# Performance work log

Measured on AMD Instinct MI355X. Metric: run time of the kernel, lower is better.

## Reference

```python
import jax, jax.numpy as jnp
import numpy as np

B, T_MEL, T_TXT = 16, 2048, 1024
D_MODEL, D_ENC_M, D_ENC_T = 512, 512, 512
LN_EPS = 1e-5


def setup_inputs() -> dict:
    key = jax.random.key(0)
    ks = jax.random.split(key, 9)
    mel_encoding = jax.random.normal(ks[0], (B, T_MEL, D_ENC_M), dtype=jnp.float32)
    text_encoding = jax.random.normal(ks[1], (B, T_TXT, D_ENC_T), dtype=jnp.float32)
    mel_mask = jax.random.randint(ks[2], (B, T_MEL), 0, 2).astype(bool)
    mel_mask = mel_mask.at[:, 0].set(False)  # guarantee >=1 unmasked key per row
    src_mask = jax.random.randint(ks[3], (B, T_TXT), 0, 2).astype(bool)
    # Projection weights stored [in, out] (torch Linear does x @ W.T)
    sc = 1.0 / np.sqrt(D_ENC_M)
    Wq = jax.random.uniform(ks[4], (D_ENC_T, D_MODEL), jnp.float32, -sc, sc)
    Wk = jax.random.uniform(ks[5], (D_ENC_M, D_MODEL), jnp.float32, -sc, sc)
    Wv = jax.random.uniform(ks[6], (D_ENC_M, D_MODEL), jnp.float32, -sc, sc)
    ln_gamma = jnp.ones((D_MODEL,), jnp.float32)
    ln_beta = jnp.zeros((D_MODEL,), jnp.float32)
    return {"mel_encoding": mel_encoding, "text_encoding": text_encoding,
            "mel_mask": mel_mask, "src_mask": src_mask,
            "Wq": Wq, "Wk": Wk, "Wv": Wv,
            "ln_gamma": ln_gamma, "ln_beta": ln_beta}


def reference(mel_encoding, text_encoding, mel_mask, src_mask, Wq, Wk, Wv, ln_gamma, ln_beta):
    temperature = jnp.sqrt(jnp.float32(D_ENC_M))
    q = jnp.einsum('btd,dm->btm', text_encoding, Wq)   # [B, T_txt, d_model]
    k = jnp.einsum('bsd,dm->bsm', mel_encoding, Wk)    # [B, T_mel, d_model]
    v = jnp.einsum('bsd,dm->bsm', mel_encoding, Wv)
    # attn_mask = outer product of src_mask and mel_mask (True -> masked)
    attn_mask = src_mask[:, :, None] & mel_mask[:, None, :]  # [B, T_txt, T_mel]
    scores = jnp.einsum('btm,bsm->bts', q, k) / temperature
    scores = jnp.where(attn_mask, -jnp.inf, scores)
    attn = jax.nn.softmax(scores, axis=2)
    output = jnp.einsum('bts,bsm->btm', attn, v)
    # dropout is identity at inference; LayerNorm over last dim
    mean = jnp.mean(output, axis=-1, keepdims=True)
    var = jnp.var(output, axis=-1, keepdims=True)
    output = (output - mean) * jax.lax.rsqrt(var + LN_EPS) * ln_gamma + ln_beta
    return output, attn
```

## Files before the change

### kernel.cpp

```cpp
#include <hip/hip_runtime.h>

#define DEV __device__ __forceinline__

typedef __attribute__((ext_vector_type(8))) short short8v;
typedef __attribute__((ext_vector_type(4))) float f32x4;

DEV unsigned short f2bf(float f) {
  unsigned int x = __float_as_uint(f);
  x = x + 0x7FFFu + ((x >> 16) & 1u);
  return (unsigned short)(x >> 16);
}
DEV float bf2f(unsigned short u) {
  return __uint_as_float(((unsigned)u) << 16);
}

DEV int swz_byte(int row, int kElem) {
  int chunk = ((kElem >> 3) ^ (row & 7));
  return row * 128 + (chunk << 4) + ((kElem & 7) << 1);
}

template <int ROUNDS>
DEV void stage(const unsigned short* __restrict__ g, int ld,
               unsigned short* tile, int tid) {
  const int wave = tid >> 6, l = tid & 63;
#pragma unroll
  for (int p = 0; p < ROUNDS; ++p) {
    const int r = (p << 5) + (wave << 3) + (l >> 3);
    const int c = ((l & 7) ^ (r & 7)) << 3;
    const unsigned short* src = g + (long)r * ld + c;
#if __has_builtin(__builtin_amdgcn_global_load_lds)
    unsigned short* dst = tile + (p << 11) + (wave << 9);
    __builtin_amdgcn_global_load_lds(
        (const __attribute__((address_space(1))) void*)src,
        (__attribute__((address_space(3))) void*)dst, 16, 0, 0);
#else
    short8v v = *reinterpret_cast<const short8v*>(src);
    *reinterpret_cast<short8v*>(reinterpret_cast<char*>(tile) +
                                (p << 12) + (wave << 10) + (l << 4)) = v;
#endif
  }
}

template <int BM, int EPI, int GM>
__global__ __launch_bounds__(256) void gemm_bf16(
    const unsigned short* __restrict__ A, const unsigned short* __restrict__ B,
    void* __restrict__ Cout, int M, int N, int K,
    long aBatch, long bBatch, long cBatch,
    const int* __restrict__ srcMask, const int* __restrict__ melMask,
    float scale, float* __restrict__ stats) {
  constexpr int NI = BM / 32;
  __shared__ unsigned short As[BM * 64];
  __shared__ unsigned short Bs[128 * 64];
  const int tid = threadIdx.x;
  const int lane = tid & 63;
  const int wave = tid >> 6;
  int z, bmi, bni;
  if constexpr (GM == 1) {
    const int id = blockIdx.x;
    z = (id & 7) | ((id >> 10) << 3);
    const int ib = (id >> 3) & 127;
    bni = ib & 15;
    bmi = ib >> 4;
  } else if constexpr (GM == 2) {
    bmi = blockIdx.x; bni = blockIdx.y; z = blockIdx.z;
  } else {
    bni = blockIdx.x; bmi = blockIdx.y; z = blockIdx.z;
  }
  const int bm = bmi * BM;
  const int bn = bni * 128;
  const unsigned short* Ab = A + (long)z * aBatch;
  const unsigned short* Bb = B + (long)z * bBatch;
  const long cOff = (long)z * cBatch;
  const int wr = (wave >> 1) * (BM / 2);
  const int wc = (wave & 1) * 64;
  const int l15 = lane & 15;
  const int lHi = lane >> 4;

  f32x4 acc[NI][4] = {};

  for (int kt = 0; kt < K; kt += 64) {
    stage<BM / 32>(Ab + (long)bm * K + kt, K, As, tid);
    stage<4>(Bb + (long)bn * K + kt, K, Bs, tid);
    __syncthreads();
#pragma unroll
    for (int ks = 0; ks < 2; ++ks) {
      const int k0 = (ks << 5) + (lHi << 3);
      short8v af[NI], bfr[4];
#pragma unroll
      for (int i = 0; i < NI; ++i)
        af[i] = *reinterpret_cast<const short8v*>(
            reinterpret_cast<const char*>(As) + swz_byte(wr + i * 16 + l15, k0));
#pragma unroll
      for (int j = 0; j < 4; ++j)
        bfr[j] = *reinterpret_cast<const short8v*>(
            reinterpret_cast<const char*>(Bs) + swz_byte(wc + j * 16 + l15, k0));
#pragma unroll
      for (int i = 0; i < NI; ++i)
#pragma unroll
        for (int j = 0; j < 4; ++j)
          acc[i][j] = __builtin_amdgcn_mfma_f32_16x16x32_bf16(af[i], bfr[j], acc[i][j], 0, 0, 0);
    }
    __syncthreads();
  }

  if constexpr (EPI >= 2) {
    __shared__ float redM[128][2];
    __shared__ float redS[128][2];
    const int wcIdx = wave & 1;
#pragma unroll
    for (int i = 0; i < NI; ++i) {
#pragma unroll
      for (int rr = 0; rr < 4; ++rr) {
        const int rloc = wr + i * 16 + lHi * 4 + rr;
        const int rb = bm + rloc;
        const bool sm = srcMask[z * 1024 + rb] != 0;
        float vals[4];
        float m_l = -3.0e38f;
#pragma unroll
        for (int j = 0; j < 4; ++j) {
          const int c = bn + wc + j * 16 + l15;
          const bool mm = melMask[z * 2048 + c] != 0;
          const float vf = (sm && mm) ? -1e30f : acc[i][j][rr] * scale;
          vals[j] = vf;
          if constexpr (EPI == 2)
            reinterpret_cast<unsigned short*>(Cout)[cOff + (long)rb * N + c] = f2bf(vf);
          else
            reinterpret_cast<float*>(Cout)[cOff + (long)rb * N + c] = vf;
          m_l = fmaxf(m_l, vf);
        }
        if (stats) {
#pragma unroll
          for (int o = 1; o < 16; o <<= 1) m_l = fmaxf(m_l, __shfl_xor(m_l, o, 64));
          float s_l = 0.f;
#pragma unroll
          for (int j = 0; j < 4; ++j) s_l += __expf(vals[j] - m_l);
#pragma unroll
          for (int o = 1; o < 16; o <<= 1) s_l += __shfl_xor(s_l, o, 64);
          if (l15 == 0) { redM[rloc][wcIdx] = m_l; redS[rloc][wcIdx] = s_l; }
        }
      }
    }
    if (stats) {
      __syncthreads();
      if (tid < 128) {
        const float m0 = redM[tid][0], m1 = redM[tid][1];
        const float Mx = fmaxf(m0, m1);
        const float S = redS[tid][0] * __expf(m0 - Mx) + redS[tid][1] * __expf(m1 - Mx);
        const long sidx = ((long)(z * 1024 + bm + tid)) * 32 + (long)bni * 2;
        stats[sidx] = Mx;
        stats[sidx + 1] = S;
      }
    }
  } else {
#pragma unroll
    for (int i = 0; i < NI; ++i) {
#pragma unroll
      for (int j = 0; j < 4; ++j) {
        const int rb = bm + wr + i * 16 + lHi * 4;
        const int c = bn + wc + j * 16 + l15;
#pragma unroll
        for (int r = 0; r < 4; ++r) {
          const float v = acc[i][j][r];
          const long idx = cOff + (long)(rb + r) * N + c;
          if constexpr (EPI == 0)
            reinterpret_cast<unsigned short*>(Cout)[idx] = f2bf(v);
          else
            reinterpret_cast<float*>(Cout)[idx] = v;
        }
      }
    }
  }
}

__global__ __launch_bounds__(256) void gemm_kv(
    const unsigned short* __restrict__ mel, const unsigned short* __restrict__ WkT,
    const unsigned short* __restrict__ WvT, unsigned short* __restrict__ kbf,
    unsigned short* __restrict__ vT) {
  __shared__ unsigned short Ms[128 * 64];
  __shared__ unsigned short Ks[128 * 64];
  __shared__ unsigned short Vs[128 * 64];
  const int id = blockIdx.x;
  const int z = (id & 7) | ((id >> 9) << 3);
  const int ib = (id >> 3) & 63;
  const int st = ib & 15, mt = ib >> 4;
  const int bs = st * 128, bmm = mt * 128;
  const int tid = threadIdx.x, lane = tid & 63, wave = tid >> 6;
  const int wrS = (wave >> 1) * 64, wcM = (wave & 1) * 64;
  const int l15 = lane & 15, lHi = lane >> 4;
  const unsigned short* melB = mel + ((long)z * 2048 + bs) * 512;

  f32x4 ak[4][4] = {};
  f32x4 av[4][4] = {};

  for (int kt = 0; kt < 512; kt += 64) {
    stage<4>(melB + kt, 512, Ms, tid);
    stage<4>(WkT + (long)bmm * 512 + kt, 512, Ks, tid);
    stage<4>(WvT + (long)bmm * 512 + kt, 512, Vs, tid);
    __syncthreads();
#pragma unroll
    for (int ks = 0; ks < 2; ++ks) {
      const int k0 = (ks << 5) + (lHi << 3);
      short8v mf[4], wf[4];
#pragma unroll
      for (int i = 0; i < 4; ++i)
        mf[i] = *reinterpret_cast<const short8v*>(
            reinterpret_cast<const char*>(Ms) + swz_byte(wrS + i * 16 + l15, k0));
#pragma unroll
      for (int j = 0; j < 4; ++j)
        wf[j] = *reinterpret_cast<const short8v*>(
            reinterpret_cast<const char*>(Ks) + swz_byte(wcM + j * 16 + l15, k0));
#pragma unroll
      for (int i = 0; i < 4; ++i)
#pragma unroll
        for (int j = 0; j < 4; ++j)
          ak[i][j] = __builtin_amdgcn_mfma_f32_16x16x32_bf16(mf[i], wf[j], ak[i][j], 0, 0, 0);
#pragma unroll
      for (int j = 0; j < 4; ++j)
        wf[j] = *reinterpret_cast<const short8v*>(
            reinterpret_cast<const char*>(Vs) + swz_byte(wcM + j * 16 + l15, k0));
#pragma unroll
      for (int i = 0; i < 4; ++i)
#pragma unroll
        for (int j = 0; j < 4; ++j)
          av[j][i] = __builtin_amdgcn_mfma_f32_16x16x32_bf16(wf[j], mf[i], av[j][i], 0, 0, 0);
    }
    __syncthreads();
  }

#pragma unroll
  for (int i = 0; i < 4; ++i)
#pragma unroll
    for (int j = 0; j < 4; ++j) {
      const int srow = bs + wrS + i * 16 + lHi * 4;
      const int mcol = bmm + wcM + j * 16 + l15;
      const int mrow = bmm + wcM + j * 16 + lHi * 4;
      const int scol = bs + wrS + i * 16 + l15;
#pragma unroll
      for (int rr = 0; rr < 4; ++rr) {
        kbf[((long)z * 2048 + srow + rr) * 512 + mcol] = f2bf(ak[i][j][rr]);
        vT[((long)z * 512 + mrow + rr) * 2048 + scol] = f2bf(av[j][i][rr]);
      }
    }
}

__global__ __launch_bounds__(256) void pv_smx(
    const unsigned short* __restrict__ sbf, const unsigned short* __restrict__ vT,
    float* __restrict__ attn, float* __restrict__ out,
    const float* __restrict__ stats) {
  __shared__ unsigned short As[64 * 64];
  __shared__ unsigned short Bs[128 * 64];
  __shared__ float rowM[64], rowInv[64];
  const int id = blockIdx.x;
  const int z = (id & 7) | ((id >> 9) << 3);
  const int ib = (id >> 3) & 63;
  const int mt = ib & 15, nt = ib >> 4;
  const int bm = mt * 64, bn = nt * 128;
  const int tid = threadIdx.x, lane = tid & 63, wave = tid >> 6;
  const bool writeAttn = (nt == 0);

  if (tid < 64) {
    const float* st = stats + ((long)(z * 1024 + bm + tid)) * 32;
    float Mx = -3.0e38f;
#pragma unroll
    for (int t = 0; t < 16; ++t) Mx = fmaxf(Mx, st[t * 2]);
    float S = 0.f;
#pragma unroll
    for (int t = 0; t < 16; ++t) S += st[t * 2 + 1] * __expf(st[t * 2] - Mx);
    rowM[tid] = Mx;
    rowInv[tid] = 1.0f / S;
  }
  __syncthreads();

  const int ar = tid >> 2;
  const int ac = (tid & 3) << 4;
  const float mR = rowM[ar];
  const float invR = rowInv[ar];
  const long aOff = ((long)z * 1024 + bm + ar) * 2048 + ac;
  const unsigned short* vTb = vT + ((long)z * 512 + bn) * 2048;
  const int wr = (wave >> 1) * 32, wc = (wave & 1) * 64;
  const int l15 = lane & 15, lHi = lane >> 4;

  f32x4 acc[2][4] = {};

  for (int kt = 0; kt < 2048; kt += 64) {
    stage<4>(vTb + kt, 2048, Bs, tid);
    const short8v s0 = *reinterpret_cast<const short8v*>(sbf + aOff + kt);
    const short8v s1 = *reinterpret_cast<const short8v*>(sbf + aOff + kt + 8);
    float e[16];
#pragma unroll
    for (int u = 0; u < 8; ++u) {
      e[u] = __expf(bf2f((unsigned short)s0[u]) - mR) * invR;
      e[u + 8] = __expf(bf2f((unsigned short)s1[u]) - mR) * invR;
    }
    if (writeAttn) {
      float* ap = attn + aOff + kt;
#pragma unroll
      for (int g = 0; g < 4; ++g) {
        float4 w;
        w.x = e[g * 4]; w.y = e[g * 4 + 1]; w.z = e[g * 4 + 2]; w.w = e[g * 4 + 3];
        *reinterpret_cast<float4*>(ap + g * 4) = w;
      }
    }
    short8v pk0, pk1;
#pragma unroll
    for (int u = 0; u < 8; ++u) {
      pk0[u] = (short)f2bf(e[u]);
      pk1[u] = (short)f2bf(e[u + 8]);
    }
    *reinterpret_cast<short8v*>(reinterpret_cast<char*>(As) + swz_byte(ar, ac)) = pk0;
    *reinterpret_cast<short8v*>(reinterpret_cast<char*>(As) + swz_byte(ar, ac + 8)) = pk1;
    __syncthreads();

#pragma unroll
    for (int ks = 0; ks < 2; ++ks) {
      const int k0 = (ks << 5) + (lHi << 3);
      short8v af[2], bfr[4];
#pragma unroll
      for (int i = 0; i < 2; ++i)
        af[i] = *reinterpret_cast<const short8v*>(
            reinterpret_cast<const char*>(As) + swz_byte(wr + i * 16 + l15, k0));
#pragma unroll
      for (int j = 0; j < 4; ++j)
        bfr[j] = *reinterpret_cast<const short8v*>(
            reinterpret_cast<const char*>(Bs) + swz_byte(wc + j * 16 + l15, k0));
#pragma unroll
      for (int i = 0; i < 2; ++i)
#pragma unroll
        for (int j = 0; j < 4; ++j)
          acc[i][j] = __builtin_amdgcn_mfma_f32_16x16x32_bf16(af[i], bfr[j], acc[i][j], 0, 0, 0);
    }
    __syncthreads();
  }

#pragma unroll
  for (int i = 0; i < 2; ++i)
#pragma unroll
    for (int j = 0; j < 4; ++j) {
      const int row = bm + wr + i * 16 + lHi * 4;
      const int col = bn + wc + j * 16 + l15;
#pragma unroll
      for (int rr = 0; rr < 4; ++rr)
        out[((long)z * 1024 + row + rr) * 512 + col] = acc[i][j][rr];
    }
}

__global__ __launch_bounds__(256) void softmax_rows(
    float* __restrict__ attn, unsigned short* __restrict__ pbf) {
  const long row = blockIdx.x;
  float4* p = reinterpret_cast<float4*>(attn + row * 2048);
  const int tid = threadIdx.x;
  float4 a = p[tid];
  float4 b = p[tid + 256];
  float m = fmaxf(fmaxf(fmaxf(a.x, a.y), fmaxf(a.z, a.w)),
                  fmaxf(fmaxf(b.x, b.y), fmaxf(b.z, b.w)));
#pragma unroll
  for (int o = 32; o; o >>= 1) m = fmaxf(m, __shfl_xor(m, o, 64));
  __shared__ float redm[4];
  if ((tid & 63) == 0) redm[tid >> 6] = m;
  __syncthreads();
  m = fmaxf(fmaxf(redm[0], redm[1]), fmaxf(redm[2], redm[3]));
  float e0 = __expf(a.x - m), e1 = __expf(a.y - m), e2 = __expf(a.z - m), e3 = __expf(a.w - m);
  float e4 = __expf(b.x - m), e5 = __expf(b.y - m), e6 = __expf(b.z - m), e7 = __expf(b.w - m);
  float s = ((e0 + e1) + (e2 + e3)) + ((e4 + e5) + (e6 + e7));
#pragma unroll
  for (int o = 32; o; o >>= 1) s += __shfl_xor(s, o, 64);
  __shared__ float reds[4];
  if ((tid & 63) == 0) reds[tid >> 6] = s;
  __syncthreads();
  s = (reds[0] + reds[1]) + (reds[2] + reds[3]);
  const float inv = 1.0f / s;
  a.x = e0 * inv; a.y = e1 * inv; a.z = e2 * inv; a.w = e3 * inv;
  b.x = e4 * inv; b.y = e5 * inv; b.z = e6 * inv; b.w = e7 * inv;
  p[tid] = a;
  p[tid + 256] = b;
  ushort4 o0, o1;
  o0.x = f2bf(a.x); o0.y = f2bf(a.y); o0.z = f2bf(a.z); o0.w = f2bf(a.w);
  o1.x = f2bf(b.x); o1.y = f2bf(b.y); o1.z = f2bf(b.z); o1.w = f2bf(b.w);
  *reinterpret_cast<ushort4*>(pbf + row * 2048 + tid * 4) = o0;
  *reinterpret_cast<ushort4*>(pbf + row * 2048 + 1024 + tid * 4) = o1;
}

__global__ __launch_bounds__(256) void f32_to_bf16(
    const float* __restrict__ in, unsigned short* __restrict__ out, long n) {
  long i = ((long)blockIdx.x * blockDim.x + threadIdx.x) * 8;
  const long stride = (long)gridDim.x * blockDim.x * 8;
  for (; i < n; i += stride) {
    const float4 a = *reinterpret_cast<const float4*>(in + i);
    const float4 b = *reinterpret_cast<const float4*>(in + i + 4);
    short8v o;
    o[0] = (short)f2bf(a.x); o[1] = (short)f2bf(a.y);
    o[2] = (short)f2bf(a.z); o[3] = (short)f2bf(a.w);
    o[4] = (short)f2bf(b.x); o[5] = (short)f2bf(b.y);
    o[6] = (short)f2bf(b.z); o[7] = (short)f2bf(b.w);
    *reinterpret_cast<short8v*>(out + i) = o;
  }
}

__global__ __launch_bounds__(256) void transpose_w3(
    const float* __restrict__ Wq, const float* __restrict__ Wk, const float* __restrict__ Wv,
    unsigned short* __restrict__ WqT, unsigned short* __restrict__ WkT,
    unsigned short* __restrict__ WvT) {
  __shared__ float t[32][33];
  const int zz = blockIdx.z;
  const float* W = zz == 0 ? Wq : zz == 1 ? Wk : Wv;
  unsigned short* WT = zz == 0 ? WqT : zz == 1 ? WkT : WvT;
  const int bx = blockIdx.x * 32;
  const int by = blockIdx.y * 32;
  const int tx = threadIdx.x, ty = threadIdx.y;
#pragma unroll
  for (int i = 0; i < 4; ++i)
    t[ty + i * 8][tx] = W[(long)(by + ty + i * 8) * 512 + bx + tx];
  __syncthreads();
#pragma unroll
  for (int i = 0; i < 4; ++i)
    WT[(long)(bx + ty + i * 8) * 512 + by + tx] = f2bf(t[tx][ty + i * 8]);
}

__global__ __launch_bounds__(64) void layernorm_rows(
    float* __restrict__ out, const float* __restrict__ gamma, const float* __restrict__ beta) {
  const long row = blockIdx.x;
  float4* p = reinterpret_cast<float4*>(out + row * 512);
  const int lane = threadIdx.x;
  float4 a = p[lane];
  float4 b = p[lane + 64];
  float s = ((a.x + a.y) + (a.z + a.w)) + ((b.x + b.y) + (b.z + b.w));
  float s2 = ((a.x * a.x + a.y * a.y) + (a.z * a.z + a.w * a.w)) +
             ((b.x * b.x + b.y * b.y) + (b.z * b.z + b.w * b.w));
#pragma unroll
  for (int o = 32; o; o >>= 1) {
    s += __shfl_xor(s, o, 64);
    s2 += __shfl_xor(s2, o, 64);
  }
  const float mean = s * (1.0f / 512.0f);
  const float var = s2 * (1.0f / 512.0f) - mean * mean;
  const float rstd = rsqrtf(var + 1e-5f);
  const float4 g0 = reinterpret_cast<const float4*>(gamma)[lane];
  const float4 g1 = reinterpret_cast<const float4*>(gamma)[lane + 64];
  const float4 c0 = reinterpret_cast<const float4*>(beta)[lane];
  const float4 c1 = reinterpret_cast<const float4*>(beta)[lane + 64];
  a.x = (a.x - mean) * rstd * g0.x + c0.x;
  a.y = (a.y - mean) * rstd * g0.y + c0.y;
  a.z = (a.z - mean) * rstd * g0.z + c0.z;
  a.w = (a.w - mean) * rstd * g0.w + c0.w;
  b.x = (b.x - mean) * rstd * g1.x + c1.x;
  b.y = (b.y - mean) * rstd * g1.y + c1.y;
  b.z = (b.z - mean) * rstd * g1.z + c1.z;
  b.w = (b.w - mean) * rstd * g1.w + c1.w;
  p[lane] = a;
  p[lane + 64] = b;
}

extern "C" void kernel_launch(void* const* d_in, const int* in_sizes, int n_in,
                              void* d_out, int out_size, void* d_ws, size_t ws_size,
                              hipStream_t stream) {
  const float* mel  = (const float*)d_in[0];
  const float* text = (const float*)d_in[1];
  const int* melMask = (const int*)d_in[2];
  const int* srcMask = (const int*)d_in[3];
  const float* Wq = (const float*)d_in[4];
  const float* Wk = (const float*)d_in[5];
  const float* Wv = (const float*)d_in[6];
  const float* gamma = (const float*)d_in[7];
  const float* beta  = (const float*)d_in[8];

  float* out = (float*)d_out;
  float* attn = (float*)d_out + (long)16 * 1024 * 512;

  unsigned short* ws = (unsigned short*)d_ws;
  unsigned short* wqT = ws;
  unsigned short* wkT = wqT + 512 * 512;
  unsigned short* wvT = wkT + 512 * 512;
  unsigned short* melbf  = wvT + 512 * 512;
  unsigned short* textbf = melbf + (long)16 * 2048 * 512;
  unsigned short* qbf = textbf + (long)16 * 1024 * 512;
  unsigned short* kbf = qbf + (long)16 * 1024 * 512;
  unsigned short* vT  = kbf + (long)16 * 2048 * 512;
  unsigned short* sbf = vT + (long)16 * 512 * 2048;
  float* stats = (float*)melbf;
  const bool bigws = ws_size >= 202899456ull;

  transpose_w3<<<dim3(16, 16, 3), dim3(32, 8), 0, stream>>>(Wq, Wk, Wv, wqT, wkT, wvT);
  f32_to_bf16<<<dim3(4096), 256, 0, stream>>>(mel, melbf, (long)16 * 2048 * 512);
  f32_to_bf16<<<dim3(2048), 256, 0, stream>>>(text, textbf, (long)16 * 1024 * 512);

  gemm_bf16<128, 0, 2><<<dim3(128, 4, 1), 256, 0, stream>>>(
      textbf, wqT, qbf, 16384, 512, 512, 0, 0, 0, nullptr, nullptr, 1.0f, nullptr);
  gemm_kv<<<dim3(1024), 256, 0, stream>>>(melbf, wkT, wvT, kbf, vT);

  if (bigws) {
    gemm_bf16<128, 2, 1><<<dim3(2048), 256, 0, stream>>>(
        qbf, kbf, sbf, 1024, 2048, 512,
        (long)1024 * 512, (long)2048 * 512, (long)1024 * 2048,
        srcMask, melMask, 0.044194173824159216f, stats);
    pv_smx<<<dim3(1024), 256, 0, stream>>>(sbf, vT, attn, out, stats);
  } else {
    unsigned short* pbf = melbf;
    gemm_bf16<128, 3, 0><<<dim3(16, 8, 16), 256, 0, stream>>>(
        qbf, kbf, attn, 1024, 2048, 512,
        (long)1024 * 512, (long)2048 * 512, (long)1024 * 2048,
        srcMask, melMask, 0.044194173824159216f, nullptr);
    softmax_rows<<<dim3(16 * 1024), 256, 0, stream>>>(attn, pbf);
    gemm_bf16<64, 1, 0><<<dim3(4, 16, 16), 256, 0, stream>>>(
        pbf, vT, out, 1024, 512, 2048,
        (long)1024 * 2048, (long)512 * 2048, (long)1024 * 512,
        nullptr, nullptr, 1.0f, nullptr);
  }
  layernorm_rows<<<dim3(16 * 1024), 64, 0, stream>>>(out, gamma, beta);
}
```

Before: 310.7 us.

## Double-buffer pv_smx tiles, spread attn writes across blocks, merge bf16 conversions

pv_smx now double-buffers the V tile and the probability tile in shared memory. The next tile's global loads and exp/bf16 packing overlap with the current tile's MFMA work, leaving one barrier per iteration. The float attn write is split among the four column-tile blocks by k-range, so nt==0 blocks no longer carry all of it. The two f32->bf16 conversion launches are fused into one. The cost is twice the LDS use, which may lower occupancy.

```diff
diff --git a/kernel.cpp b/kernel.cpp
--- a/kernel.cpp
+++ b/kernel.cpp
@@ -247,8 +247,8 @@
     const unsigned short* __restrict__ sbf, const unsigned short* __restrict__ vT,
     float* __restrict__ attn, float* __restrict__ out,
     const float* __restrict__ stats) {
-  __shared__ unsigned short As[64 * 64];
-  __shared__ unsigned short Bs[128 * 64];
+  __shared__ unsigned short As[2][64 * 64];
+  __shared__ unsigned short Bs[2][128 * 64];
   __shared__ float rowM[64], rowInv[64];
   const int id = blockIdx.x;
   const int z = (id & 7) | ((id >> 9) << 3);
@@ -256,7 +256,6 @@
   const int mt = ib & 15, nt = ib >> 4;
   const int bm = mt * 64, bn = nt * 128;
   const int tid = threadIdx.x, lane = tid & 63, wave = tid >> 6;
-  const bool writeAttn = (nt == 0);
 
   if (tid < 64) {
     const float* st = stats + ((long)(z * 1024 + bm + tid)) * 32;
@@ -281,18 +280,20 @@
   const int l15 = lane & 15, lHi = lane >> 4;
 
   f32x4 acc[2][4] = {};
-
-  for (int kt = 0; kt < 2048; kt += 64) {
-    stage<4>(vTb + kt, 2048, Bs, tid);
-    const short8v s0 = *reinterpret_cast<const short8v*>(sbf + aOff + kt);
-    const short8v s1 = *reinterpret_cast<const short8v*>(sbf + aOff + kt + 8);
+  short8v s0, s1;
+
+  auto loadS = [&](int kt) {
+    s0 = *reinterpret_cast<const short8v*>(sbf + aOff + kt);
+    s1 = *reinterpret_cast<const short8v*>(sbf + aOff + kt + 8);
+  };
+  auto computeA = [&](int kt, unsigned short* AsB) {
     float e[16];
 #pragma unroll
     for (int u = 0; u < 8; ++u) {
       e[u] = __expf(bf2f((unsigned short)s0[u]) - mR) * invR;
       e[u + 8] = __expf(bf2f((unsigned short)s1[u]) - mR) * invR;
     }
-    if (writeAttn) {
+    if ((kt >> 9) == nt) {
       float* ap = attn + aOff + kt;
 #pragma unroll
       for (int g = 0; g < 4; ++g) {
@@ -307,10 +308,25 @@
       pk0[u] = (short)f2bf(e[u]);
       pk1[u] = (short)f2bf(e[u + 8]);
     }
-    *reinterpret_cast<short8v*>(reinterpret_cast<char*>(As) + swz_byte(ar, ac)) = pk0;
-    *reinterpret_cast<short8v*>(reinterpret_cast<char*>(As) + swz_byte(ar, ac + 8)) = pk1;
-    __syncthreads();
-
+    *reinterpret_cast<short8v*>(reinterpret_cast<char*>(AsB) + swz_byte(ar, ac)) = pk0;
+    *reinterpret_cast<short8v*>(reinterpret_cast<char*>(AsB) + swz_byte(ar, ac + 8)) = pk1;
+  };
+
+  stage<4>(vTb, 2048, Bs[0], tid);
+  loadS(0);
+  computeA(0, As[0]);
+  asm volatile("s_waitcnt vmcnt(0) lgkmcnt(0)" ::: "memory");
+  __builtin_amdgcn_s_barrier();
+  __builtin_amdgcn_sched_barrier(0);
+
+  for (int t = 0; t < 32; ++t) {
+    const int c = t & 1;
+    if (t < 31) {
+      stage<4>(vTb + (t + 1) * 64, 2048, Bs[c ^ 1], tid);
+      loadS((t + 1) * 64);
+    }
+    const unsigned short* AsC = As[c];
+    const unsigned short* BsC = Bs[c];
 #pragma unroll
     for (int ks = 0; ks < 2; ++ks) {
       const int k0 = (ks << 5) + (lHi << 3);
@@ -318,18 +334,21 @@
 #pragma unroll
       for (int i = 0; i < 2; ++i)
         af[i] = *reinterpret_cast<const short8v*>(
-            reinterpret_cast<const char*>(As) + swz_byte(wr + i * 16 + l15, k0));
+            reinterpret_cast<const char*>(AsC) + swz_byte(wr + i * 16 + l15, k0));
 #pragma unroll
       for (int j = 0; j < 4; ++j)
         bfr[j] = *reinterpret_cast<const short8v*>(
-            reinterpret_cast<const char*>(Bs) + swz_byte(wc + j * 16 + l15, k0));
+            reinterpret_cast<const char*>(BsC) + swz_byte(wc + j * 16 + l15, k0));
 #pragma unroll
       for (int i = 0; i < 2; ++i)
 #pragma unroll
         for (int j = 0; j < 4; ++j)
           acc[i][j] = __builtin_amdgcn_mfma_f32_16x16x32_bf16(af[i], bfr[j], acc[i][j], 0, 0, 0);
     }
-    __syncthreads();
+    if (t < 31) computeA((t + 1) * 64, As[c ^ 1]);
+    asm volatile("s_waitcnt vmcnt(0) lgkmcnt(0)" ::: "memory");
+    __builtin_amdgcn_s_barrier();
+    __builtin_amdgcn_sched_barrier(0);
   }
 
 #pragma unroll
@@ -380,19 +399,23 @@
   *reinterpret_cast<ushort4*>(pbf + row * 2048 + 1024 + tid * 4) = o1;
 }
 
-__global__ __launch_bounds__(256) void f32_to_bf16(
-    const float* __restrict__ in, unsigned short* __restrict__ out, long n) {
+__global__ __launch_bounds__(256) void f32_to_bf16_2(
+    const float* __restrict__ inA, unsigned short* __restrict__ outA, long nA,
+    const float* __restrict__ inB, unsigned short* __restrict__ outB, long nB) {
+  const long total = nA + nB;
   long i = ((long)blockIdx.x * blockDim.x + threadIdx.x) * 8;
   const long stride = (long)gridDim.x * blockDim.x * 8;
-  for (; i < n; i += stride) {
-    const float4 a = *reinterpret_cast<const float4*>(in + i);
-    const float4 b = *reinterpret_cast<const float4*>(in + i + 4);
+  for (; i < total; i += stride) {
+    const float* in = (i < nA) ? inA + i : inB + (i - nA);
+    unsigned short* out = (i < nA) ? outA + i : outB + (i - nA);
+    const float4 a = *reinterpret_cast<const float4*>(in);
+    const float4 b = *reinterpret_cast<const float4*>(in + 4);
     short8v o;
     o[0] = (short)f2bf(a.x); o[1] = (short)f2bf(a.y);
     o[2] = (short)f2bf(a.z); o[3] = (short)f2bf(a.w);
     o[4] = (short)f2bf(b.x); o[5] = (short)f2bf(b.y);
     o[6] = (short)f2bf(b.z); o[7] = (short)f2bf(b.w);
-    *reinterpret_cast<short8v*>(out + i) = o;
+    *reinterpret_cast<short8v*>(out) = o;
   }
 }
 
@@ -480,8 +503,8 @@
   const bool bigws = ws_size >= 202899456ull;
 
   transpose_w3<<<dim3(16, 16, 3), dim3(32, 8), 0, stream>>>(Wq, Wk, Wv, wqT, wkT, wvT);
-  f32_to_bf16<<<dim3(4096), 256, 0, stream>>>(mel, melbf, (long)16 * 2048 * 512);
-  f32_to_bf16<<<dim3(2048), 256, 0, stream>>>(text, textbf, (long)16 * 1024 * 512);
+  f32_to_bf16_2<<<dim3(6144), 256, 0, stream>>>(
+      mel, melbf, (long)16 * 2048 * 512, text, textbf, (long)16 * 1024 * 512);
 
   gemm_bf16<128, 0, 2><<<dim3(128, 4, 1), 256, 0, stream>>>(
       textbf, wqT, qbf, 16384, 512, 512, 0, 0, 0, nullptr, nullptr, 1.0f, nullptr);
```

Measured after the change: 336.6 us. 8.3% more time.
